# Kernel tuning notes

Measured on AMD Instinct MI355X. Metric: run time of the kernel, lower is better.

Reference implementation:

```python
import jax, jax.numpy as jnp
import numpy as np

DMODEL = 1024
N_EXPERTS = 8
EXPERT_SIZE = 4096
TOPK = 2
B, S = 2, 2048


def setup_inputs() -> dict:
    key = jax.random.key(0)
    ks = jax.random.split(key, 6)
    std = EXPERT_SIZE ** (-0.5)  # init_expert_weights: normal(0, expert_size**-0.5 * weight_scale)
    x = jax.random.normal(ks[0], (B, S, DMODEL), dtype=jnp.float32)
    gate_w = 0.02 * jax.random.normal(ks[1], (N_EXPERTS, DMODEL), dtype=jnp.float32)
    w1 = std * jax.random.normal(ks[2], (N_EXPERTS, EXPERT_SIZE, DMODEL), dtype=jnp.float32)
    b1 = jnp.zeros((N_EXPERTS, EXPERT_SIZE), dtype=jnp.float32)
    w2 = std * jax.random.normal(ks[3], (N_EXPERTS, DMODEL, EXPERT_SIZE), dtype=jnp.float32)
    b2 = jnp.zeros((N_EXPERTS, DMODEL), dtype=jnp.float32)
    return {"x": x, "gate_w": gate_w, "w1": w1, "b1": b1, "w2": w2, "b2": b2}


def reference(x, gate_w, w1, b1, w2, b2):
    # Router: gate linear (no bias) -> softmax -> top-k expert selection
    logits = jnp.einsum('bsd,ed->bse', x, gate_w)          # [B,S,E]
    probs = jax.nn.softmax(logits, axis=-1)                # gate_softmax
    top_w, top_i = jax.lax.top_k(probs, TOPK)              # [B,S,K]
    # Scatter top-k weights back to a dense [B,S,E] routing matrix
    route = jnp.sum(jax.nn.one_hot(top_i, N_EXPERTS, dtype=probs.dtype)
                    * top_w[..., None], axis=-2)           # [B,S,E]
    # Per-expert 2-layer MLP (Linear -> ReLU -> Linear), combined by route weights
    out = jnp.zeros_like(x)
    for e in range(N_EXPERTS):
        h = jax.nn.relu(jnp.einsum('bsd,hd->bsh', x, w1[e]) + b1[e])  # [B,S,H]
        y = jnp.einsum('bsh,dh->bsd', h, w2[e]) + b2[e]               # [B,S,D]
        out = out + route[..., e, None] * y
    return out
```

## Files before the change

### kernel.cpp

```cpp
#include <hip/hip_runtime.h>
#include <hip/hip_bf16.h>
#include <stdint.h>

#define DMODEL 1024
#define NEXP   8
#define HSZ    4096
#define NTOK   4096

typedef __attribute__((ext_vector_type(8))) short bf16x8;
typedef __attribute__((ext_vector_type(4))) float f32x4;

__device__ __forceinline__ unsigned short f2bf(float f) {
  union { float f; unsigned u; } v; v.f = f;
  return (unsigned short)((v.u + 0x8000u) >> 16);
}

__device__ __forceinline__ void gl2lds16(const void* g, void* lds) {
  __builtin_amdgcn_global_load_lds(
      (const __attribute__((address_space(1))) unsigned*)g,
      (__attribute__((address_space(3))) unsigned*)lds, 16, 0, 0);
}

__global__ __launch_bounds__(256) void cvt_all_kernel(
    const float* __restrict__ x, const float* __restrict__ w1,
    const float* __restrict__ w2, unsigned short* __restrict__ xb,
    unsigned short* __restrict__ w1b, unsigned short* __restrict__ w2b) {
  const size_t n0 = (size_t)NTOK * DMODEL / 4;
  const size_t n1 = (size_t)NEXP * HSZ * DMODEL / 4;
  size_t i = (size_t)blockIdx.x * 256 + threadIdx.x;
  const float* src; unsigned short* dst; size_t j;
  if (i < n0)            { src = x;  dst = xb;  j = i; }
  else if (i < n0 + n1)  { src = w1; dst = w1b; j = i - n0; }
  else                   { src = w2; dst = w2b; j = i - n0 - n1; }
  float4 v = ((const float4*)src)[j];
  ((ushort4*)dst)[j] = make_ushort4(f2bf(v.x), f2bf(v.y), f2bf(v.z), f2bf(v.w));
}

__global__ __launch_bounds__(256) void router_kernel(
    const float* __restrict__ x, const float* __restrict__ gw,
    int* __restrict__ cnt, int* __restrict__ tokl, float* __restrict__ twgt,
    int* __restrict__ sidx) {
  int wave = threadIdx.x >> 6;
  int lane = threadIdx.x & 63;
  int t = blockIdx.x * 4 + wave;
  const float* xr = x + (size_t)t * DMODEL;
  float acc[NEXP];
#pragma unroll
  for (int e = 0; e < NEXP; ++e) acc[e] = 0.f;
  for (int d = lane; d < DMODEL; d += 64) {
    float xv = xr[d];
#pragma unroll
    for (int e = 0; e < NEXP; ++e) acc[e] = fmaf(xv, gw[e * DMODEL + d], acc[e]);
  }
#pragma unroll
  for (int e = 0; e < NEXP; ++e) {
#pragma unroll
    for (int o = 32; o > 0; o >>= 1) acc[e] += __shfl_down(acc[e], o);
  }
  if (lane == 0) {
    float m = acc[0];
#pragma unroll
    for (int e = 1; e < NEXP; ++e) m = fmaxf(m, acc[e]);
    float p[NEXP]; float s = 0.f;
#pragma unroll
    for (int e = 0; e < NEXP; ++e) { p[e] = __expf(acc[e] - m); s += p[e]; }
    float inv = 1.f / s;
    int i0 = 0; float b0 = p[0];
#pragma unroll
    for (int e = 1; e < NEXP; ++e) if (p[e] > b0) { b0 = p[e]; i0 = e; }
    int i1 = (i0 == 0) ? 1 : 0; float b1v = p[i1];
#pragma unroll
    for (int e = 0; e < NEXP; ++e) if (e != i0 && p[e] > b1v) { b1v = p[e]; i1 = e; }
    int p0 = atomicAdd(&cnt[i0], 1);
    tokl[i0 * NTOK + p0] = t; twgt[i0 * NTOK + p0] = b0 * inv;
    int p1 = atomicAdd(&cnt[i1], 1);
    tokl[i1 * NTOK + p1] = t; twgt[i1 * NTOK + p1] = b1v * inv;
    sidx[2 * t]     = (i0 << 16) | p0;
    sidx[2 * t + 1] = (i1 << 16) | p1;
  }
}

__global__ __launch_bounds__(256) void gemm1_bf_kernel(
    const unsigned short* __restrict__ Xbf, const unsigned short* __restrict__ W1bf,
    const float* __restrict__ b1, const int* __restrict__ cnt,
    const int* __restrict__ tokl, unsigned short* __restrict__ Hbuf) {
  const int e = blockIdx.z;
  const int ne = cnt[e];
  const int m0 = blockIdx.y * 128;
  if (m0 >= ne) return;
  const int n0 = blockIdx.x * 128;
  int toff = 0;
  for (int i = 0; i < NEXP; ++i) toff += (i < e) ? cnt[i] : 0;

  __shared__ __align__(16) unsigned short As[128 * 32];
  __shared__ __align__(16) unsigned short Bs[128 * 32];

  const int tid = threadIdx.x;
  const int lane = tid & 63;
  const int wave = tid >> 6;
  const int wm = (wave >> 1) * 64;
  const int wn = (wave & 1) * 64;

  const int srow = wave * 16 + (lane >> 2);
  const int scol = (lane & 3) * 8;
  const int* tlist = tokl + e * NTOK;
  const unsigned short* gA[2]; const unsigned short* gB[2];
  unsigned short* lA[2]; unsigned short* lB[2];
#pragma unroll
  for (int c = 0; c < 2; ++c) {
    int r = c * 64 + srow;
    int gr = m0 + r;
    int tk = tlist[(gr < ne) ? gr : 0];
    gA[c] = Xbf + (size_t)tk * DMODEL + scol;
    gB[c] = W1bf + (size_t)e * HSZ * DMODEL + (size_t)(n0 + r) * DMODEL + scol;
    lA[c] = &As[(c * 64 + wave * 16) * 32];
    lB[c] = &Bs[(c * 64 + wave * 16) * 32];
  }

  f32x4 acc[4][4];
#pragma unroll
  for (int i = 0; i < 4; ++i)
#pragma unroll
    for (int j = 0; j < 4; ++j) acc[i][j] = (f32x4){0.f, 0.f, 0.f, 0.f};

  const int fr = lane & 15;
  const int fk = (lane >> 4) * 8;

  for (int k0 = 0; k0 < DMODEL; k0 += 32) {
    __syncthreads();
#pragma unroll
    for (int c = 0; c < 2; ++c) {
      gl2lds16(gA[c] + k0, lA[c]);
      gl2lds16(gB[c] + k0, lB[c]);
    }
    __syncthreads();
    bf16x8 af[4], bfg[4];
#pragma unroll
    for (int i = 0; i < 4; ++i) {
      af[i]  = *(const bf16x8*)&As[(wm + i * 16 + fr) * 32 + fk];
      bfg[i] = *(const bf16x8*)&Bs[(wn + i * 16 + fr) * 32 + fk];
    }
#pragma unroll
    for (int i = 0; i < 4; ++i)
#pragma unroll
      for (int j = 0; j < 4; ++j)
        acc[i][j] = __builtin_amdgcn_mfma_f32_16x16x32_bf16(bfg[j], af[i], acc[i][j], 0, 0, 0);
  }

  const int hq = (lane >> 4) * 4;
#pragma unroll
  for (int i = 0; i < 4; ++i) {
    int trow = m0 + wm + i * 16 + fr;
    if (trow >= ne) continue;
    size_t hrow = (size_t)(toff + trow) * HSZ;
#pragma unroll
    for (int j = 0; j < 4; ++j) {
      int hcol = n0 + wn + j * 16 + hq;
      const float* bp = b1 + e * HSZ + hcol;
      unsigned short u[4];
#pragma unroll
      for (int r = 0; r < 4; ++r)
        u[r] = f2bf(fmaxf(acc[i][j][r] + bp[r], 0.f));
      *(ushort4*)&Hbuf[hrow + hcol] = make_ushort4(u[0], u[1], u[2], u[3]);
    }
  }
}

__global__ __launch_bounds__(256) void gemm2_bf_kernel(
    const unsigned short* __restrict__ Hbuf, const unsigned short* __restrict__ W2bf,
    const float* __restrict__ b2, const int* __restrict__ cnt,
    const float* __restrict__ twgt, float* __restrict__ Ybuf) {
  const int e = blockIdx.z;
  const int ne = cnt[e];
  const int m0 = blockIdx.y * 128;
  if (m0 >= ne) return;
  const int n0 = blockIdx.x * 128;
  int toff = 0;
  for (int i = 0; i < NEXP; ++i) toff += (i < e) ? cnt[i] : 0;

  __shared__ __align__(16) unsigned short As[128 * 64];
  __shared__ __align__(16) unsigned short Bs[128 * 64];

  const int tid = threadIdx.x;
  const int lane = tid & 63;
  const int wave = tid >> 6;
  const int wm = (wave >> 1) * 64;
  const int wn = (wave & 1) * 64;

  const int srow = (wave << 5) + (lane >> 3);
  const int scb  = (((lane & 7) ^ (lane >> 3)) << 3);
  const unsigned short* gA[4]; const unsigned short* gB[4];
  unsigned short* lA[4]; unsigned short* lB[4];
#pragma unroll
  for (int c = 0; c < 4; ++c) {
    int r = srow + c * 8;
    int gr = m0 + r;
    int rc = (gr < ne) ? gr : 0;
    gA[c] = Hbuf + (size_t)(toff + rc) * HSZ + scb;
    gB[c] = W2bf + (size_t)e * DMODEL * HSZ + (size_t)(n0 + r) * HSZ + scb;
    lA[c] = &As[((wave << 5) + c * 8) * 64];
    lB[c] = &Bs[((wave << 5) + c * 8) * 64];
  }

  f32x4 acc[4][4];
#pragma unroll
  for (int i = 0; i < 4; ++i)
#pragma unroll
    for (int j = 0; j < 4; ++j) acc[i][j] = (f32x4){0.f, 0.f, 0.f, 0.f};

  const int fr = lane & 15;
  const int cb0 = lane >> 4;

  for (int k0 = 0; k0 < HSZ; k0 += 64) {
    __syncthreads();
#pragma unroll
    for (int c = 0; c < 4; ++c) {
      gl2lds16(gA[c] + k0, lA[c]);
      gl2lds16(gB[c] + k0, lB[c]);
    }
    __syncthreads();
    bf16x8 af[2][4], bfg[2][4];
#pragma unroll
    for (int h = 0; h < 2; ++h) {
      int cb = cb0 + h * 4;
#pragma unroll
      for (int i = 0; i < 4; ++i) {
        int ar = wm + i * 16 + fr;
        af[h][i]  = *(const bf16x8*)&As[ar * 64 + ((cb ^ (ar & 7)) << 3)];
        int br = wn + i * 16 + fr;
        bfg[h][i] = *(const bf16x8*)&Bs[br * 64 + ((cb ^ (br & 7)) << 3)];
      }
    }
#pragma unroll
    for (int h = 0; h < 2; ++h)
#pragma unroll
      for (int i = 0; i < 4; ++i)
#pragma unroll
        for (int j = 0; j < 4; ++j)
          acc[i][j] = __builtin_amdgcn_mfma_f32_16x16x32_bf16(bfg[h][j], af[h][i],
                                                              acc[i][j], 0, 0, 0);
  }

  const float* wlist = twgt + e * NTOK;
  const int dq = (lane >> 4) * 4;
#pragma unroll
  for (int i = 0; i < 4; ++i) {
    int trow = m0 + wm + i * 16 + fr;
    if (trow >= ne) continue;
    float wgt = wlist[trow];
    float* yrow = Ybuf + (size_t)(toff + trow) * DMODEL;
#pragma unroll
    for (int j = 0; j < 4; ++j) {
      int d0 = n0 + wn + j * 16 + dq;
      const float* b2p = b2 + e * DMODEL + d0;
      float4 v = make_float4(wgt * (acc[i][j][0] + b2p[0]),
                             wgt * (acc[i][j][1] + b2p[1]),
                             wgt * (acc[i][j][2] + b2p[2]),
                             wgt * (acc[i][j][3] + b2p[3]));
      *(float4*)(yrow + d0) = v;
    }
  }
}

__global__ __launch_bounds__(256) void combine_kernel(
    const float* __restrict__ Ybuf, const int* __restrict__ cnt,
    const int* __restrict__ sidx, float* __restrict__ out) {
  int t = blockIdx.x;
  int offv[NEXP];
  int s = 0;
#pragma unroll
  for (int e = 0; e < NEXP; ++e) { offv[e] = s; s += cnt[e]; }
  int s0 = sidx[2 * t], s1 = sidx[2 * t + 1];
  size_t r0 = (size_t)(offv[s0 >> 16] + (s0 & 0xffff)) * DMODEL;
  size_t r1 = (size_t)(offv[s1 >> 16] + (s1 & 0xffff)) * DMODEL;
  int c = threadIdx.x * 4;
  float4 a = *(const float4*)(Ybuf + r0 + c);
  float4 b = *(const float4*)(Ybuf + r1 + c);
  *(float4*)(out + (size_t)t * DMODEL + c) =
      make_float4(a.x + b.x, a.y + b.y, a.z + b.z, a.w + b.w);
}

extern "C" void kernel_launch(void* const* d_in, const int* in_sizes, int n_in,
                              void* d_out, int out_size, void* d_ws, size_t ws_size,
                              hipStream_t stream) {
  const float* x  = (const float*)d_in[0];
  const float* gw = (const float*)d_in[1];
  const float* w1 = (const float*)d_in[2];
  const float* b1 = (const float*)d_in[3];
  const float* w2 = (const float*)d_in[4];
  const float* b2 = (const float*)d_in[5];
  float* out = (float*)d_out;

  char* ws = (char*)d_ws;
  int* cnt    = (int*)ws;
  int* tokl   = (int*)(ws + 128);
  float* twgt = (float*)(ws + 128 + NEXP * NTOK * 4);
  int* sidx   = (int*)(ws + 128 + 2 * NEXP * NTOK * 4);

  constexpr size_t OFF_XBF  = 327680;
  constexpr size_t OFF_W1BF = OFF_XBF  + (size_t)NTOK * DMODEL * 2;
  constexpr size_t OFF_W2BF = OFF_W1BF + (size_t)NEXP * HSZ * DMODEL * 2;
  constexpr size_t OFF_HBUF = OFF_W2BF + (size_t)NEXP * DMODEL * HSZ * 2;
  unsigned short* Xbf  = (unsigned short*)(ws + OFF_XBF);
  unsigned short* W1bf = (unsigned short*)(ws + OFF_W1BF);
  unsigned short* W2bf = (unsigned short*)(ws + OFF_W2BF);
  unsigned short* Hbuf = (unsigned short*)(ws + OFF_HBUF);
  float* Ybuf = (float*)(ws + OFF_W1BF);

  hipMemsetAsync(cnt, 0, 32, stream);
  router_kernel<<<NTOK / 4, 256, 0, stream>>>(x, gw, cnt, tokl, twgt, sidx);
  const size_t ncvt = (size_t)NTOK * DMODEL / 4 + 2 * (size_t)NEXP * HSZ * DMODEL / 4;
  cvt_all_kernel<<<(unsigned)((ncvt + 255) / 256), 256, 0, stream>>>(
      x, w1, w2, Xbf, W1bf, W2bf);
  gemm1_bf_kernel<<<dim3(HSZ / 128, NTOK / 128, NEXP), 256, 0, stream>>>(
      Xbf, W1bf, b1, cnt, tokl, Hbuf);
  gemm2_bf_kernel<<<dim3(DMODEL / 128, NTOK / 128, NEXP), 256, 0, stream>>>(
      Hbuf, W2bf, b2, cnt, twgt, Ybuf);
  combine_kernel<<<NTOK, 256, 0, stream>>>(Ybuf, cnt, sidx, out);
}
```

Before: 665.8 us.

## Split-K gemm2 into two partial buffers and widen gemm1 K-tile with swizzled LDS

Widens gemm1's K step from 32 to 64, using the XOR-swizzled LDS layout already used in gemm2. This halves the number of barrier pairs per tile and cuts LDS bank conflicts. Splits gemm2's 4096-long K reduction across two blocks, which doubles the grid (gemm2 otherwise launches few blocks). Each half writes to its own fp32 partial buffer and the combine kernel sums both. The cost is extra Y write and read traffic, and the relocated Ybuf now overlaps the Xbf and W1bf region, which is safe only because gemm1 has already finished.

Result: slower. 692.9 us (+4.1%).

```diff
diff --git a/kernel.cpp b/kernel.cpp
--- a/kernel.cpp
+++ b/kernel.cpp
@@ -6,6 +6,8 @@
 #define NEXP   8
 #define HSZ    4096
 #define NTOK   4096
+#define NROWS  (2 * NTOK)
+#define SK2    2
 
 typedef __attribute__((ext_vector_type(8))) short bf16x8;
 typedef __attribute__((ext_vector_type(4))) float f32x4;
@@ -92,8 +94,8 @@
   int toff = 0;
   for (int i = 0; i < NEXP; ++i) toff += (i < e) ? cnt[i] : 0;
 
-  __shared__ __align__(16) unsigned short As[128 * 32];
-  __shared__ __align__(16) unsigned short Bs[128 * 32];
+  __shared__ __align__(16) unsigned short As[128 * 64];
+  __shared__ __align__(16) unsigned short Bs[128 * 64];
 
   const int tid = threadIdx.x;
   const int lane = tid & 63;
@@ -101,20 +103,20 @@
   const int wm = (wave >> 1) * 64;
   const int wn = (wave & 1) * 64;
 
-  const int srow = wave * 16 + (lane >> 2);
-  const int scol = (lane & 3) * 8;
+  const int srow = (wave << 5) + (lane >> 3);
+  const int scb  = (((lane & 7) ^ (lane >> 3)) << 3);
   const int* tlist = tokl + e * NTOK;
-  const unsigned short* gA[2]; const unsigned short* gB[2];
-  unsigned short* lA[2]; unsigned short* lB[2];
-#pragma unroll
-  for (int c = 0; c < 2; ++c) {
-    int r = c * 64 + srow;
+  const unsigned short* gA[4]; const unsigned short* gB[4];
+  unsigned short* lA[4]; unsigned short* lB[4];
+#pragma unroll
+  for (int c = 0; c < 4; ++c) {
+    int r = srow + c * 8;
     int gr = m0 + r;
     int tk = tlist[(gr < ne) ? gr : 0];
-    gA[c] = Xbf + (size_t)tk * DMODEL + scol;
-    gB[c] = W1bf + (size_t)e * HSZ * DMODEL + (size_t)(n0 + r) * DMODEL + scol;
-    lA[c] = &As[(c * 64 + wave * 16) * 32];
-    lB[c] = &Bs[(c * 64 + wave * 16) * 32];
+    gA[c] = Xbf + (size_t)tk * DMODEL + scb;
+    gB[c] = W1bf + (size_t)e * HSZ * DMODEL + (size_t)(n0 + r) * DMODEL + scb;
+    lA[c] = &As[((wave << 5) + c * 8) * 64];
+    lB[c] = &Bs[((wave << 5) + c * 8) * 64];
   }
 
   f32x4 acc[4][4];
@@ -124,27 +126,36 @@
     for (int j = 0; j < 4; ++j) acc[i][j] = (f32x4){0.f, 0.f, 0.f, 0.f};
 
   const int fr = lane & 15;
-  const int fk = (lane >> 4) * 8;
-
-  for (int k0 = 0; k0 < DMODEL; k0 += 32) {
+  const int cb0 = lane >> 4;
+
+  for (int k0 = 0; k0 < DMODEL; k0 += 64) {
     __syncthreads();
 #pragma unroll
-    for (int c = 0; c < 2; ++c) {
+    for (int c = 0; c < 4; ++c) {
       gl2lds16(gA[c] + k0, lA[c]);
       gl2lds16(gB[c] + k0, lB[c]);
     }
     __syncthreads();
-    bf16x8 af[4], bfg[4];
-#pragma unroll
-    for (int i = 0; i < 4; ++i) {
-      af[i]  = *(const bf16x8*)&As[(wm + i * 16 + fr) * 32 + fk];
-      bfg[i] = *(const bf16x8*)&Bs[(wn + i * 16 + fr) * 32 + fk];
-    }
-#pragma unroll
-    for (int i = 0; i < 4; ++i)
-#pragma unroll
-      for (int j = 0; j < 4; ++j)
-        acc[i][j] = __builtin_amdgcn_mfma_f32_16x16x32_bf16(bfg[j], af[i], acc[i][j], 0, 0, 0);
+    bf16x8 af[2][4], bfg[2][4];
+#pragma unroll
+    for (int h = 0; h < 2; ++h) {
+      int cb = cb0 + h * 4;
+#pragma unroll
+      for (int i = 0; i < 4; ++i) {
+        int ar = wm + i * 16 + fr;
+        af[h][i]  = *(const bf16x8*)&As[ar * 64 + ((cb ^ (ar & 7)) << 3)];
+        int br = wn + i * 16 + fr;
+        bfg[h][i] = *(const bf16x8*)&Bs[br * 64 + ((cb ^ (br & 7)) << 3)];
+      }
+    }
+#pragma unroll
+    for (int h = 0; h < 2; ++h)
+#pragma unroll
+      for (int i = 0; i < 4; ++i)
+#pragma unroll
+        for (int j = 0; j < 4; ++j)
+          acc[i][j] = __builtin_amdgcn_mfma_f32_16x16x32_bf16(bfg[h][j], af[h][i],
+                                                              acc[i][j], 0, 0, 0);
   }
 
   const int hq = (lane >> 4) * 4;
@@ -174,7 +185,9 @@
   const int ne = cnt[e];
   const int m0 = blockIdx.y * 128;
   if (m0 >= ne) return;
-  const int n0 = blockIdx.x * 128;
+  const int n0 = (blockIdx.x & 7) * 128;
+  const int kz = blockIdx.x >> 3;
+  const int kbase = kz * (HSZ / SK2);
   int toff = 0;
   for (int i = 0; i < NEXP; ++i) toff += (i < e) ? cnt[i] : 0;
 
@@ -211,7 +224,7 @@
   const int fr = lane & 15;
   const int cb0 = lane >> 4;
 
-  for (int k0 = 0; k0 < HSZ; k0 += 64) {
+  for (int k0 = kbase; k0 < kbase + HSZ / SK2; k0 += 64) {
     __syncthreads();
 #pragma unroll
     for (int c = 0; c < 4; ++c) {
@@ -243,20 +256,24 @@
 
   const float* wlist = twgt + e * NTOK;
   const int dq = (lane >> 4) * 4;
+  float* ybase = Ybuf + (size_t)kz * NROWS * DMODEL;
 #pragma unroll
   for (int i = 0; i < 4; ++i) {
     int trow = m0 + wm + i * 16 + fr;
     if (trow >= ne) continue;
     float wgt = wlist[trow];
-    float* yrow = Ybuf + (size_t)(toff + trow) * DMODEL;
+    float* yrow = ybase + (size_t)(toff + trow) * DMODEL;
 #pragma unroll
     for (int j = 0; j < 4; ++j) {
       int d0 = n0 + wn + j * 16 + dq;
       const float* b2p = b2 + e * DMODEL + d0;
-      float4 v = make_float4(wgt * (acc[i][j][0] + b2p[0]),
-                             wgt * (acc[i][j][1] + b2p[1]),
-                             wgt * (acc[i][j][2] + b2p[2]),
-                             wgt * (acc[i][j][3] + b2p[3]));
+      float4 v;
+      if (kz == 0)
+        v = make_float4(wgt * (acc[i][j][0] + b2p[0]), wgt * (acc[i][j][1] + b2p[1]),
+                        wgt * (acc[i][j][2] + b2p[2]), wgt * (acc[i][j][3] + b2p[3]));
+      else
+        v = make_float4(wgt * acc[i][j][0], wgt * acc[i][j][1],
+                        wgt * acc[i][j][2], wgt * acc[i][j][3]);
       *(float4*)(yrow + d0) = v;
     }
   }
@@ -273,11 +290,15 @@
   int s0 = sidx[2 * t], s1 = sidx[2 * t + 1];
   size_t r0 = (size_t)(offv[s0 >> 16] + (s0 & 0xffff)) * DMODEL;
   size_t r1 = (size_t)(offv[s1 >> 16] + (s1 & 0xffff)) * DMODEL;
+  const float* Y1 = Ybuf + (size_t)NROWS * DMODEL;
   int c = threadIdx.x * 4;
   float4 a = *(const float4*)(Ybuf + r0 + c);
   float4 b = *(const float4*)(Ybuf + r1 + c);
+  float4 a2 = *(const float4*)(Y1 + r0 + c);
+  float4 b2 = *(const float4*)(Y1 + r1 + c);
   *(float4*)(out + (size_t)t * DMODEL + c) =
-      make_float4(a.x + b.x, a.y + b.y, a.z + b.z, a.w + b.w);
+      make_float4(a.x + b.x + a2.x + b2.x, a.y + b.y + a2.y + b2.y,
+                  a.z + b.z + a2.z + b2.z, a.w + b.w + a2.w + b2.w);
 }
 
 extern "C" void kernel_launch(void* const* d_in, const int* in_sizes, int n_in,
@@ -305,7 +326,7 @@
   unsigned short* W1bf = (unsigned short*)(ws + OFF_W1BF);
   unsigned short* W2bf = (unsigned short*)(ws + OFF_W2BF);
   unsigned short* Hbuf = (unsigned short*)(ws + OFF_HBUF);
-  float* Ybuf = (float*)(ws + OFF_W1BF);
+  float* Ybuf = (float*)(ws + OFF_XBF);
 
   hipMemsetAsync(cnt, 0, 32, stream);
   router_kernel<<<NTOK / 4, 256, 0, stream>>>(x, gw, cnt, tokl, twgt, sidx);
@@ -314,7 +335,7 @@
       x, w1, w2, Xbf, W1bf, W2bf);
   gemm1_bf_kernel<<<dim3(HSZ / 128, NTOK / 128, NEXP), 256, 0, stream>>>(
       Xbf, W1bf, b1, cnt, tokl, Hbuf);
-  gemm2_bf_kernel<<<dim3(DMODEL / 128, NTOK / 128, NEXP), 256, 0, stream>>>(
+  gemm2_bf_kernel<<<dim3(8 * SK2, NTOK / 128, NEXP), 256, 0, stream>>>(
       Hbuf, W2bf, b2, cnt, twgt, Ybuf);
   combine_kernel<<<NTOK, 256, 0, stream>>>(Ybuf, cnt, sidx, out);
 }
```
